# Performance work log

Hardware: AMD Instinct MI355X
Metric: run time of the kernel (lower is better)

The kernel has to match this reference:

```python
import jax, jax.numpy as jnp
import numpy as np
from jax import lax

Z_MAX = 0.3
WAVELENGTHS = jnp.array([0.65, 0.53, 0.47], jnp.float32)
LUMA = jnp.array([0.299, 0.587, 0.114], jnp.float32)


def conv2d(x, w, b):
    # x: (B,C,H,W), w: (O,I,kh,kw), SAME padding, stride 1
    y = lax.conv_general_dilated(x, w, (1, 1), 'SAME',
                                 dimension_numbers=('NCHW', 'OIHW', 'NCHW'))
    return y + b[None, :, None, None]


def group_norm(x, g, b, eps=1e-5):
    # GroupNorm(num_groups=1): normalize over (C,H,W) per sample
    mu = x.mean(axis=(1, 2, 3), keepdims=True)
    var = ((x - mu) ** 2).mean(axis=(1, 2, 3), keepdims=True)
    xn = (x - mu) * lax.rsqrt(var + eps)
    return xn * g[None, :, None, None] + b[None, :, None, None]


def setup_inputs() -> dict:
    key = jax.random.key(0)
    ks = jax.random.split(key, 16)
    B, C, H, W = 8, 3, 512, 512
    PH, ZH, MH = 16, 16, 32
    s = 0.1
    inp = {
        'x': jax.random.uniform(ks[0], (B, C, H, W), jnp.float32),
        'norm_g': jnp.ones((C,), jnp.float32), 'norm_b': jnp.zeros((C,), jnp.float32),
        'ph_w1': jax.random.normal(ks[1], (PH, C, 3, 3), jnp.float32) * s,
        'ph_b1': jnp.zeros((PH,), jnp.float32),
        'ph_w2': jax.random.normal(ks[2], (C, PH, 3, 3), jnp.float32) * s,
        'ph_b2': jnp.zeros((C,), jnp.float32),
        'z_w1': jax.random.normal(ks[3], (ZH, C, 3, 3), jnp.float32) * s,
        'z_b1': jnp.zeros((ZH,), jnp.float32),
        'z_w2': jax.random.normal(ks[4], (C, ZH, 3, 3), jnp.float32) * s,
        'z_b2': jnp.zeros((C,), jnp.float32),
        'freq_gain': jax.random.normal(ks[5], (C,), jnp.float32) * 0.01,
        'mix_w1': jax.random.normal(ks[6], (MH, C + 2, 3, 3), jnp.float32) * s,
        'mix_b1': jnp.zeros((MH,), jnp.float32),
        'gn1_g': jnp.ones((MH,), jnp.float32), 'gn1_b': jnp.zeros((MH,), jnp.float32),
        'mix_w2': jax.random.normal(ks[7], (MH, MH, 3, 3), jnp.float32) * s,
        'mix_b2': jnp.zeros((MH,), jnp.float32),
        'gn2_g': jnp.ones((MH,), jnp.float32), 'gn2_b': jnp.zeros((MH,), jnp.float32),
        'mix_w3': jax.random.normal(ks[8], (C, MH, 1, 1), jnp.float32) * s,
        'mix_b3': jnp.zeros((C,), jnp.float32),
        'se_w1': jax.random.normal(ks[9], (4, C), jnp.float32) * s,   # mid = max(3//4,4)=4
        'se_b1': jnp.zeros((4,), jnp.float32),
        'se_w2': jax.random.normal(ks[10], (C, 4), jnp.float32) * s,
        'se_b2': jnp.zeros((C,), jnp.float32),
        'alpha': jnp.asarray(0.3, jnp.float32),
    }
    return inp


def reference(x, norm_g, norm_b, ph_w1, ph_b1, ph_w2, ph_b2,
              z_w1, z_b1, z_w2, z_b2, freq_gain,
              mix_w1, mix_b1, gn1_g, gn1_b, mix_w2, mix_b2, gn2_g, gn2_b,
              mix_w3, mix_b3, se_w1, se_b1, se_w2, se_b2, alpha):
    B, C, H, W = x.shape
    # 1) norm
    xn = group_norm(x, norm_g, norm_b)
    # 2) phase prediction (small CNN, phi in [-pi, pi])
    h = jax.nn.silu(conv2d(xn, ph_w1, ph_b1))
    phi = jnp.tanh(conv2d(h, ph_w2, ph_b2)) * jnp.pi
    # 3) per-pixel propagation distance z in [0, z_max]
    hz = jax.nn.silu(conv2d(xn, z_w1, z_b1))
    z = jax.nn.sigmoid(conv2d(hz, z_w2, z_b2)) * Z_MAX
    # 4) complex field U0 = amp * exp(i*phi)  (amp_mode='identity')
    U0 = lax.complex(x * jnp.cos(phi), x * jnp.sin(phi))
    # 5) ASM propagation. kz = 2*pi*sqrt(1/lam^2 - fx^2 - fy^2), per-channel wavelength.
    fy = jnp.fft.fftfreq(H).astype(jnp.float32)
    fx = jnp.fft.fftfreq(W).astype(jnp.float32)
    f2 = fy[:, None] ** 2 + fx[None, :] ** 2                     # (H,W)
    inv_l2 = (1.0 / WAVELENGTHS ** 2)[:, None, None]             # (3,1,1)
    kz = 2.0 * jnp.pi * jnp.sqrt(jnp.maximum(inv_l2 - f2[None], 0.0))  # (3,H,W)
    # spatially varying z: base propagation at mean z + spatial phase correction
    z_mean = z.mean(axis=(2, 3), keepdims=True)                  # (B,3,1,1)
    Uf = jnp.fft.fft2(U0)
    Uf = Uf * (1.0 + freq_gain)[None, :, None, None].astype(Uf.dtype)  # FreqEnhance gain
    hp = kz[None] * z_mean                                       # (B,3,H,W)
    Uz = jnp.fft.ifft2(Uf * lax.complex(jnp.cos(hp), jnp.sin(hp)))
    k0 = (2.0 * jnp.pi / WAVELENGTHS)[None, :, None, None]
    cp = k0 * (z - z_mean)
    Uz = Uz * lax.complex(jnp.cos(cp), jnp.sin(cp))
    # 6) J = |Uz| with clamped sqrt
    J = jnp.sqrt(jnp.maximum(Uz.real ** 2 + Uz.imag ** 2, 1e-12))
    # 7) mix head: [x, J_luma, J_contrast] -> delta
    lw = LUMA[None, :, None, None]
    x_l = (x * lw).sum(axis=1, keepdims=True)
    J_l = (J * lw).sum(axis=1, keepdims=True)
    mix_in = jnp.concatenate([x, J_l, J_l - x_l], axis=1)        # (B,5,H,W)
    d = jax.nn.silu(group_norm(conv2d(mix_in, mix_w1, mix_b1), gn1_g, gn1_b))
    d = jax.nn.silu(group_norm(conv2d(d, mix_w2, mix_b2), gn2_g, gn2_b))
    delta = conv2d(d, mix_w3, mix_b3)                            # (B,3,H,W)
    # 8) SE channel attention
    p = delta.mean(axis=(2, 3))                                  # (B,3)
    wse = jax.nn.sigmoid(jax.nn.silu(p @ se_w1.T + se_b1) @ se_w2.T + se_b2)
    delta = delta * wse[:, :, None, None]
    # 9) residual update
    return x + alpha * delta
```

## Files before the change

### kernel.cpp

```cpp
#include <hip/hip_runtime.h>
#include <hip/hip_bf16.h>
#include <math.h>

#define DINL __device__ __forceinline__

namespace {
constexpr int Bn = 8, Cn = 3, Hn = 512, Wn = 512;
constexpr int HW  = Hn * Wn;
constexpr int CHW = Cn * HW;
constexpr float GEPS = 1e-5f;
constexpr float PIf  = 3.14159265358979323846f;

constexpr size_t OFF_RED = 0;
constexpr size_t OFF_PHI = 512;
constexpr size_t OFF_U   = OFF_PHI + (size_t)Bn * CHW * 2;
constexpr size_t OFF_J   = OFF_U   + (size_t)Bn * CHW * 4;
constexpr size_t OFF_D   = OFF_J   + (size_t)Bn * CHW * 2;
constexpr size_t OFF_Y2  = OFF_D   + (size_t)Bn * CHW * 2;
constexpr size_t OFF_W1B = OFF_Y2  + (size_t)Bn * 32 * HW;
constexpr size_t OFF_W2F = OFF_W1B + 3072 * 2;
constexpr size_t OFF_WH1 = OFF_W2F + 9216;
constexpr size_t OFF_WP2 = OFF_WH1 + 4608 * 2;
constexpr size_t OFF_WZ2 = OFF_WP2 + 4608;
constexpr size_t OFF_PRM = OFF_WZ2 + 4608;
constexpr size_t OFF_PART= OFF_PRM + 160 * 4;
constexpr size_t OFF_TW  = OFF_PART + 81920 * 4;
constexpr int PZ = 0;
constexpr int PG1 = 24576;
constexpr int PG2 = 40960;
constexpr int PD  = 57344;
}

typedef __bf16 bfx8 __attribute__((ext_vector_type(8)));
typedef float  fx4  __attribute__((ext_vector_type(4)));
typedef float  fx2  __attribute__((ext_vector_type(2)));

DINL float frcp(float a) { return __builtin_amdgcn_rcpf(a); }
DINL float sigm(float a) { return frcp(1.f + __expf(-a)); }
DINL float siluf(float a) { return a * frcp(1.f + __expf(-a)); }
DINL float ftanh(float a) { return 1.f - 2.f * frcp(1.f + __expf(2.f * a)); }
DINL unsigned short f2bf(float f) {
    unsigned u = __float_as_uint(f);
    return (unsigned short)((u + 0x7FFFu + ((u >> 16) & 1u)) >> 16);
}
DINL float bf2f(unsigned short h) {
    return __uint_as_float(((unsigned)h) << 16);
}
DINL unsigned short t1(float a) { return (unsigned short)(__float_as_uint(a) >> 16); }
DINL unsigned t2(float a, float b) {
    return (__float_as_uint(a) >> 16) | (__float_as_uint(b) & 0xFFFF0000u);
}
DINL unsigned char f2f8(float v) {
    return (unsigned char)(__builtin_amdgcn_cvt_pk_fp8_f32(v, v, 0, false) & 0xFF);
}
DINL unsigned short pk8(float a, float b) {
    return (unsigned short)(__builtin_amdgcn_cvt_pk_fp8_f32(a, b, 0, false) & 0xFFFF);
}
DINL unsigned pk4f8(float a, float b, float c, float d) {
    unsigned u = __builtin_amdgcn_cvt_pk_fp8_f32(a, b, 0, false);
    u = __builtin_amdgcn_cvt_pk_fp8_f32(c, d, u, true);
    return u;
}
template<int SEL>
DINL float f8f(unsigned u) { return __builtin_amdgcn_cvt_f32_fp8(u, SEL); }
DINL unsigned pkh(float a, float b) {
    auto h = __builtin_amdgcn_cvt_pkrtz(a, b);
    unsigned u; __builtin_memcpy(&u, &h, 4); return u;
}
DINL float2 uph(unsigned u) {
    _Float16 h[2]; __builtin_memcpy(h, &u, 4);
    return make_float2((float)h[0], (float)h[1]);
}
DINL unsigned short f2h(float a) {
    _Float16 h = (_Float16)a; unsigned short s; __builtin_memcpy(&s, &h, 2); return s;
}
DINL float h2f(unsigned short s) {
    _Float16 h; __builtin_memcpy(&h, &s, 2); return (float)h;
}

DINL int SW(int e) { return e ^ ((e >> 4) & 7); }

DINL float blockReduceSum(float v) {
    __shared__ float sm[4];
    int lane = threadIdx.x & 63, wid = threadIdx.x >> 6;
    #pragma unroll
    for (int o = 32; o > 0; o >>= 1) v += __shfl_down(v, o, 64);
    __syncthreads();
    if (lane == 0) sm[wid] = v;
    __syncthreads();
    if (wid == 0) {
        float r = (lane < 4) ? sm[lane] : 0.f;
        r += __shfl_down(r, 2, 64);
        r += __shfl_down(r, 1, 64);
        return r;
    }
    return 0.f;
}

DINL void blockReduceSum3(float& a, float& b, float& c) {
    __shared__ float sm3[12];
    int lane = threadIdx.x & 63, wid = threadIdx.x >> 6;
    #pragma unroll
    for (int o = 32; o > 0; o >>= 1) {
        a += __shfl_down(a, o, 64);
        b += __shfl_down(b, o, 64);
        c += __shfl_down(c, o, 64);
    }
    __syncthreads();
    if (lane == 0) { sm3[wid] = a; sm3[4 + wid] = b; sm3[8 + wid] = c; }
    __syncthreads();
    if (threadIdx.x == 0) {
        a = sm3[0] + sm3[1] + sm3[2] + sm3[3];
        b = sm3[4] + sm3[5] + sm3[6] + sm3[7];
        c = sm3[8] + sm3[9] + sm3[10] + sm3[11];
    }
}

__global__ __launch_bounds__(256) void k_init(
    const float* __restrict__ w1, const float* __restrict__ w2,
    const float* __restrict__ phw1, const float* __restrict__ zw1,
    const float* __restrict__ phw2, const float* __restrict__ zw2,
    const float* __restrict__ g2g, const float* __restrict__ g2b,
    const float* __restrict__ w3,
    unsigned short* __restrict__ w1bf, unsigned char* __restrict__ w2f8,
    unsigned short* __restrict__ wh1, unsigned char* __restrict__ wp2,
    unsigned char* __restrict__ wz2, float* __restrict__ prm,
    float2* __restrict__ gtw,
    const float* __restrict__ x, float* __restrict__ part)
{
    if (blockIdx.x < 36) {
        int i = blockIdx.x * 256 + threadIdx.x;
        if (i < 3072) {
            int o = i / 96, k = i - o * 96;
            int ky = k >> 5, r = k & 31, kx = r >> 3, c = r & 7;
            float v = 0.f;
            if (kx < 3 && c < 4) {
                float base = w1[o * 45 + c * 9 + ky * 3 + kx];
                float w4   = w1[o * 45 + 4 * 9 + ky * 3 + kx];
                v = (c == 3) ? base + w4
                  : base - ((c == 0) ? 0.299f : (c == 1) ? 0.587f : 0.114f) * w4;
            }
            w1bf[i] = f2bf(v);
        }
        if (i < 9216) {
            int tap = i >> 10, rr = i & 1023, row = rr >> 5, ci = rr & 31;
            int n = row & 15, hi = row >> 4;
            int ch = (n >> 2) * 8 + hi * 4 + (n & 3);
            w2f8[i] = f2f8(w2[ch * 288 + ci * 9 + tap]);
        }
        if (i < 4608) {
            int o = i / 96, k = i - o * 96;
            int ky = k >> 5, r = k & 31, kx = r >> 3, c = r & 7;
            float v = 0.f;
            if (kx < 3 && c < 3)
                v = (o < 16) ? phw1[o * 27 + c * 9 + ky * 3 + kx]
                             : zw1[(o - 16) * 27 + c * 9 + ky * 3 + kx];
            wh1[i] = f2bf(v);
        }
        if (i < 4608) {
            int tap = i / 512, rr = i - tap * 512, n = rr >> 5, k = rr & 31;
            float vp = (n < 3 && k < 16) ? phw2[n * 144 + k * 9 + tap] : 0.f;
            float vz = (n < 3) ? zw2[n * 288 + k * 9 + tap] : 0.f;
            wp2[i] = f2f8(vp);
            wz2[i] = f2f8(vz);
        }
        if (i < 160) {
            if (i < 32) {
                prm[i] = g2g[i];
            } else if (i < 64) {
                prm[i] = g2b[i - 32];
            } else {
                int j = (i - 64) & 31, c = (i - 64) >> 5;
                prm[i] = w3[c * 32 + j];
            }
        }
        return;
    }
    if (blockIdx.x == 36) {
        for (int i = threadIdx.x; i < 512; i += 256) {
            float s, c; __sincosf(-2.f * PIf * (float)i * (1.f / 512.f), &s, &c);
            gtw[i] = make_float2(c, s);
        }
        return;
    }
    const int bid = blockIdx.x - 37;
    const int b = bid >> 5, blk = bid & 31;
    const float4* xv = (const float4*)(x + (size_t)b * CHW + (size_t)blk * (CHW / 32));
    float s = 0.f, ss = 0.f;
    for (int i = threadIdx.x; i < (CHW / 32) / 4; i += 256) {
        float4 v = xv[i];
        s  += v.x + v.y + v.z + v.w;
        ss += v.x * v.x + v.y * v.y + v.z * v.z + v.w * v.w;
    }
    float rs = blockReduceSum(s);
    float rss = blockReduceSum(ss);
    if (threadIdx.x == 0) {
        part[PG1 + b * 64 + blk] = rs;
        part[PG1 + b * 64 + 32 + blk] = rss;
    }
}

__global__ __launch_bounds__(256) void k_heads(
    const float* __restrict__ x,
    const float* __restrict__ ng, const float* __restrict__ nb,
    const unsigned short* __restrict__ wh1,
    const float* __restrict__ phb1, const float* __restrict__ zb1,
    const unsigned char* __restrict__ wp2, const unsigned char* __restrict__ wz2,
    const float* __restrict__ phb2, const float* __restrict__ zb2,
    unsigned short* __restrict__ phi, float* __restrict__ part)
{
    const int tx0 = blockIdx.x * 16, ty0 = blockIdx.y * 16, b = blockIdx.z;
    const int local = blockIdx.y * 32 + blockIdx.x;
    const bool edge = (blockIdx.x == 0) || (blockIdx.x == 31) ||
                      (blockIdx.y == 0) || (blockIdx.y == 31);
    __shared__ unsigned short mt8[20 * 21 * 8];
    __shared__ __attribute__((aligned(16))) unsigned char ht8[324 * 48];
    __shared__ float xst[2];
    const int t = threadIdx.x;
    {
        const float* px = part + PG1 + (size_t)b * 64;
        float sv  = (t < 32) ? px[t] : 0.f;
        float ssv = (t >= 32 && t < 64) ? px[t] : 0.f;
        float r0 = blockReduceSum(sv);
        float r1 = blockReduceSum(ssv);
        if (t == 0) { xst[0] = r0; xst[1] = r1; }
        __syncthreads();
    }
    const float mu = xst[0] * (1.f / CHW);
    const float rsv = rsqrtf(xst[1] * (1.f / CHW) - mu * mu + GEPS);
    float sc[3], sh[3];
    #pragma unroll
    for (int c = 0; c < 3; ++c) { sc[c] = rsv * ng[c]; sh[c] = nb[c] - mu * rsv * ng[c]; }
    if (edge) {
        for (int e = t; e < 20 * 21; e += 256) {
            int yy = e / 21, xx = e - yy * 21;
            int gy = ty0 - 2 + yy, gx = tx0 - 2 + xx;
            float v0 = 0, v1 = 0, v2 = 0;
            if (xx < 20 && (unsigned)gy < (unsigned)Hn && (unsigned)gx < (unsigned)Wn) {
                size_t p = (size_t)b * CHW + (size_t)gy * Wn + gx;
                v0 = x[p] * sc[0] + sh[0];
                v1 = x[p + HW] * sc[1] + sh[1];
                v2 = x[p + 2 * HW] * sc[2] + sh[2];
            }
            *(uint4*)(mt8 + e * 8) = make_uint4(t2(v0, v1), (unsigned)t1(v2), 0u, 0u);
        }
    } else {
        for (int e = t; e < 20 * 21; e += 256) {
            int yy = e / 21, xx = e - yy * 21;
            float v0 = 0, v1 = 0, v2 = 0;
            if (xx < 20) {
                size_t p = (size_t)b * CHW + (size_t)(ty0 - 2 + yy) * Wn + (tx0 - 2 + xx);
                v0 = x[p] * sc[0] + sh[0];
                v1 = x[p + HW] * sc[1] + sh[1];
                v2 = x[p + 2 * HW] * sc[2] + sh[2];
            }
            *(uint4*)(mt8 + e * 8) = make_uint4(t2(v0, v1), (unsigned)t1(v2), 0u, 0u);
        }
    }
    const int wv = t >> 6, lane = t & 63, ln = lane & 15, q = lane >> 4;
    bfx8 Bf[3][3];
    #pragma unroll
    for (int ks = 0; ks < 3; ++ks)
        #pragma unroll
        for (int nt = 0; nt < 3; ++nt)
            Bf[ks][nt] = *(const bfx8*)(wh1 + (nt * 16 + ln) * 96 + ks * 32 + q * 8);
    float bph[4], bz0[4], bz1[4];
    #pragma unroll
    for (int r = 0; r < 4; ++r) {
        int ch = q * 4 + r;
        bph[r] = phb1[ch]; bz0[r] = zb1[ch]; bz1[r] = zb1[16 + ch];
    }
    __syncthreads();
    for (int mt = wv; mt < 21; mt += 4) {
        int p = mt * 16 + ln; if (p > 323) p = 323;
        const int hy = p / 18, hx = p - hy * 18;
        fx4 a0 = {0,0,0,0}, a1 = {0,0,0,0}, a2 = {0,0,0,0};
        #pragma unroll
        for (int ks = 0; ks < 3; ++ks) {
            bfx8 A = *(const bfx8*)(mt8 + ((hy + ks) * 21 + hx + q) * 8);
            a0 = __builtin_amdgcn_mfma_f32_16x16x32_bf16(Bf[ks][0], A, a0, 0, 0, 0);
            a1 = __builtin_amdgcn_mfma_f32_16x16x32_bf16(Bf[ks][1], A, a1, 0, 0, 0);
            a2 = __builtin_amdgcn_mfma_f32_16x16x32_bf16(Bf[ks][2], A, a2, 0, 0, 0);
        }
        bool live = true;
        if (edge) {
            const int gy = ty0 - 1 + hy, gx = tx0 - 1 + hx;
            live = (unsigned)gy < (unsigned)Hn && (unsigned)gx < (unsigned)Wn;
        }
        unsigned d0 = pk4f8(siluf(a0[0] + bph[0]), siluf(a0[1] + bph[1]),
                            siluf(a0[2] + bph[2]), siluf(a0[3] + bph[3]));
        unsigned d1 = pk4f8(siluf(a1[0] + bz0[0]), siluf(a1[1] + bz0[1]),
                            siluf(a1[2] + bz0[2]), siluf(a1[3] + bz0[3]));
        unsigned d2 = pk4f8(siluf(a2[0] + bz1[0]), siluf(a2[1] + bz1[1]),
                            siluf(a2[2] + bz1[2]), siluf(a2[3] + bz1[3]));
        if (!live) { d0 = 0u; d1 = 0u; d2 = 0u; }
        unsigned* hp = (unsigned*)(ht8 + p * 48 + q * 4);
        hp[0] = d0; hp[4] = d1; hp[8] = d2;
    }
    __syncthreads();
    fx4 accp[4], accz[4];
    #pragma unroll
    for (int i = 0; i < 4; ++i) { accp[i] = fx4{0,0,0,0}; accz[i] = fx4{0,0,0,0}; }
    #pragma unroll
    for (int tap = 0; tap < 9; ++tap) {
        const int ky = tap / 3, kx = tap - ky * 3;
        long Bp = *(const long*)(wp2 + tap * 512 + ln * 32 + q * 8);
        long Bz = *(const long*)(wz2 + tap * 512 + ln * 32 + q * 8);
        #pragma unroll
        for (int i = 0; i < 4; ++i) {
            const int oy = wv * 4 + i;
            const unsigned char* ap = ht8 + ((oy + ky) * 18 + ln + kx) * 48;
            long Ap = *(const long*)(ap + q * 8);
            long Az = *(const long*)(ap + 16 + q * 8);
            accp[i] = __builtin_amdgcn_mfma_f32_16x16x32_fp8_fp8(Ap, Bp, accp[i], 0, 0, 0);
            accz[i] = __builtin_amdgcn_mfma_f32_16x16x32_fp8_fp8(Az, Bz, accz[i], 0, 0, 0);
        }
    }
    __syncthreads();
    float* phs = (float*)ht8;
    float* zs  = phs + 1024;
    if (ln < 3) {
        #pragma unroll
        for (int i = 0; i < 4; ++i)
            #pragma unroll
            for (int r = 0; r < 4; ++r) {
                int pl = (wv * 4 + i) * 16 + q * 4 + r;
                phs[pl * 4 + ln] = accp[i][r];
                zs [pl * 4 + ln] = accz[i][r];
            }
    }
    asm volatile("" ::: "memory");
    float4 pv = ((const float4*)phs)[t];
    float4 zv = ((const float4*)zs)[t];
    const int gy = ty0 + (t >> 4), gx = tx0 + (t & 15);
    size_t pp = (size_t)b * CHW + (size_t)gy * Wn + gx;
    phi[pp]          = f2h(ftanh(pv.x + phb2[0]) * PIf);
    phi[pp + HW]     = f2h(ftanh(pv.y + phb2[1]) * PIf);
    phi[pp + 2 * HW] = f2h(ftanh(pv.z + phb2[2]) * PIf);
    float z0 = sigm(zv.x + zb2[0]) * 0.3f;
    float z1 = sigm(zv.y + zb2[1]) * 0.3f;
    float z2 = sigm(zv.z + zb2[2]) * 0.3f;
    blockReduceSum3(z0, z1, z2);
    if (t == 0) {
        part[PZ + (size_t)(b * 3 + 0) * 1024 + local] = z0;
        part[PZ + (size_t)(b * 3 + 1) * 1024 + local] = z1;
        part[PZ + (size_t)(b * 3 + 2) * 1024 + local] = z2;
    }
}

template<bool INV>
DINL float2* fft512_wave4(float2* a, float2* b, const float2* tw, int l)
{
    float2* src = a; float2* dst = b;
    int s = 1;
    #pragma unroll
    for (int st = 0; st < 4; ++st) {
        #pragma unroll
        for (int h = 0; h < 2; ++h) {
            const int i = l + h * 64;
            const int q = i & (s - 1);
            const int sm = i - q;
            const int si = SW(i);
            float2 A = src[si], B = src[si + 128], C = src[si + 256], D = src[si + 384];
            float t0x = A.x + C.x, t0y = A.y + C.y;
            float t1x = A.x - C.x, t1y = A.y - C.y;
            float t2x = B.x + D.x, t2y = B.y + D.y;
            float t3x = B.x - D.x, t3y = B.y - D.y;
            float i3x = INV ? -t3y : t3y;
            float i3y = INV ? t3x : -t3x;
            float u0x = t0x + t2x, u0y = t0y + t2y;
            float u2x = t0x - t2x, u2y = t0y - t2y;
            float u1x = t1x + i3x, u1y = t1y + i3y;
            float u3x = t1x - i3x, u3y = t1y - i3y;
            float2 w1 = tw[SW(sm)], w2 = tw[SW(2 * sm)], w3 = tw[SW(3 * sm)];
            float w1y = INV ? -w1.y : w1.y;
            float w2y = INV ? -w2.y : w2.y;
            float w3y = INV ? -w3.y : w3.y;
            const int base = q + 4 * sm;
            dst[SW(base)]         = make_float2(u0x, u0y);
            dst[SW(base + s)]     = make_float2(u1x * w1.x - u1y * w1y, u1x * w1y + u1y * w1.x);
            dst[SW(base + 2 * s)] = make_float2(u2x * w2.x - u2y * w2y, u2x * w2y + u2y * w2.x);
            dst[SW(base + 3 * s)] = make_float2(u3x * w3.x - u3y * w3y, u3x * w3y + u3y * w3.x);
        }
        float2* tmp = src; src = dst; dst = tmp;
        s <<= 2;
        asm volatile("" ::: "memory");
    }
    #pragma unroll
    for (int h = 0; h < 4; ++h) {
        const int j = l + h * 64;
        const int sj = SW(j);
        float2 u = src[sj], v = src[sj + 256];
        dst[sj]       = make_float2(u.x + v.x, u.y + v.y);
        dst[sj + 256] = make_float2(u.x - v.x, u.y - v.y);
    }
    float2* tmp = src; src = dst; dst = tmp;
    asm volatile("" ::: "memory");
    return src;
}

__global__ __launch_bounds__(256) void k_fftA(
    const float* __restrict__ x, const unsigned short* __restrict__ phi,
    unsigned* __restrict__ U, const float2* __restrict__ gtw)
{
    __shared__ float2 buf[4][2][512];
    __shared__ float2 tw[512];
    const int t = threadIdx.x, wv = t >> 6, l = t & 63;
    #pragma unroll
    for (int i = t; i < 512; i += 256) tw[SW(i)] = gtw[i];
    __syncthreads();
    const size_t line = (size_t)blockIdx.x * 4 + wv;
    const float* xr = x + line * 512;
    const unsigned short* pr = phi + line * 512;
    float2* A = buf[wv][0];
    float2* B = buf[wv][1];
    #pragma unroll
    for (int i = l; i < 512; i += 64) {
        float s, c; __sincosf(h2f(pr[i]), &s, &c);
        float xv = xr[i];
        A[SW(i)] = make_float2(xv * c, xv * s);
    }
    asm volatile("" ::: "memory");
    float2* res = fft512_wave4<false>(A, B, tw, l);
    unsigned* Ur = U + line * 512;
    #pragma unroll
    for (int i = l; i < 512; i += 64) {
        float2 v = res[SW(i)];
        Ur[i] = pkh(v.x, v.y);
    }
}

__global__ __launch_bounds__(256) void k_transpose(unsigned* __restrict__ U,
                                                   const float* __restrict__ part,
                                                   float* __restrict__ red)
{
    const int img = blockIdx.y;
    if (blockIdx.x == 0) {
        float4 a4 = ((const float4*)(part + PZ + (size_t)img * 1024))[threadIdx.x];
        float r = blockReduceSum(a4.x + a4.y + a4.z + a4.w);
        if (threadIdx.x == 0) red[16 + img] = r;
    }
    int rem = blockIdx.x, ti = 0;
    while (rem >= 8 - ti) { rem -= 8 - ti; ++ti; }
    const int tj = ti + rem;
    unsigned* Ub = U + (size_t)img * HW;
    __shared__ unsigned ta[64][65];
    __shared__ unsigned tb[64][65];
    const int t = threadIdx.x;
    const int cc = t & 63, r0 = t >> 6;
    const int ar = ti * 64, ac = tj * 64;
    #pragma unroll
    for (int k = 0; k < 16; ++k) {
        int r = r0 + k * 4;
        ta[r][cc] = Ub[(size_t)(ar + r) * 512 + ac + cc];
    }
    if (ti != tj) {
        #pragma unroll
        for (int k = 0; k < 16; ++k) {
            int r = r0 + k * 4;
            tb[r][cc] = Ub[(size_t)(ac + r) * 512 + ar + cc];
        }
    }
    __syncthreads();
    #pragma unroll
    for (int k = 0; k < 16; ++k) {
        int r = r0 + k * 4;
        Ub[(size_t)(ac + r) * 512 + ar + cc] = ta[cc][r];
    }
    if (ti != tj) {
        #pragma unroll
        for (int k = 0; k < 16; ++k) {
            int r = r0 + k * 4;
            Ub[(size_t)(ar + r) * 512 + ac + cc] = tb[cc][r];
        }
    }
}

__global__ __launch_bounds__(256) void k_fftB(
    unsigned* __restrict__ U, const float* __restrict__ red,
    const float* __restrict__ fgain, const float2* __restrict__ gtw)
{
    __shared__ float2 buf[4][2][512];
    __shared__ float2 tw[512];
    const int t = threadIdx.x, wv = t >> 6, l = t & 63;
    #pragma unroll
    for (int i = t; i < 512; i += 256) tw[SW(i)] = gtw[i];
    const int line = blockIdx.x * 4 + wv;
    const int bc = line >> 9;
    const int fw = line & 511;
    const int c = bc % 3;
    const float zm = red[16 + bc] * (1.f / HW);
    __syncthreads();
    unsigned* Ur = U + (size_t)line * 512;
    float2* A = buf[wv][0];
    float2* B = buf[wv][1];
    #pragma unroll
    for (int i = l; i < 512; i += 64) A[SW(i)] = uph(Ur[i]);
    asm volatile("" ::: "memory");
    float2* res = fft512_wave4<false>(A, B, tw, l);
    const float gain = 1.f + fgain[c];
    const float lam  = (c == 0) ? 0.65f : (c == 1) ? 0.53f : 0.47f;
    const float il2  = 1.f / (lam * lam);
    const float fwv  = (float)(fw < 256 ? fw : fw - 512) * (1.f / 512.f);
    const float f2w  = fwv * fwv;
    #pragma unroll
    for (int i = l; i < 512; i += 64) {
        float fh = (float)(i < 256 ? i : i - 512) * (1.f / 512.f);
        float kz = 2.f * PIf * sqrtf(fmaxf(il2 - f2w - fh * fh, 0.f));
        float sn, cs; __sincosf(kz * zm, &sn, &cs);
        const int si = SW(i);
        float2 v = res[si];
        res[si] = make_float2(gain * (v.x * cs - v.y * sn), gain * (v.x * sn + v.y * cs));
    }
    asm volatile("" ::: "memory");
    float2* other = (res == A) ? B : A;
    float2* res2 = fft512_wave4<true>(res, other, tw, l);
    #pragma unroll
    for (int i = l; i < 512; i += 64) {
        float2 v = res2[SW(i)];
        Ur[i] = pkh(v.x * (1.f / 512.f), v.y * (1.f / 512.f));
    }
}

__global__ __launch_bounds__(256) void k_fftC(
    const unsigned* __restrict__ U, unsigned short* __restrict__ J,
    const float2* __restrict__ gtw)
{
    __shared__ float2 buf[4][2][512];
    __shared__ float2 tw[512];
    const int t = threadIdx.x, wv = t >> 6, l = t & 63;
    #pragma unroll
    for (int i = t; i < 512; i += 256) tw[SW(i)] = gtw[i];
    __syncthreads();
    const size_t line = (size_t)blockIdx.x * 4 + wv;
    const unsigned* Ur = U + line * 512;
    float2* A = buf[wv][0];
    float2* B = buf[wv][1];
    #pragma unroll
    for (int i = l; i < 512; i += 64) A[SW(i)] = uph(Ur[i]);
    asm volatile("" ::: "memory");
    float2* res = fft512_wave4<true>(A, B, tw, l);
    unsigned short* Jr = J + line * 512;
    #pragma unroll
    for (int i = l; i < 512; i += 64) {
        float2 v = res[SW(i)];
        float re = v.x * (1.f / 512.f), im = v.y * (1.f / 512.f);
        Jr[i] = f2h(sqrtf(fmaxf(re * re + im * im, 1e-12f)));
    }
}

__global__ __launch_bounds__(256) void k_m1(
    const float* __restrict__ x, const unsigned short* __restrict__ Jb,
    const unsigned short* __restrict__ w1bf, const float* __restrict__ b1,
    float* __restrict__ part)
{
    const int tx0 = blockIdx.x * 32, ty0 = blockIdx.y * 32, b = blockIdx.z;
    const int local = blockIdx.y * 16 + blockIdx.x;
    const bool edge = (blockIdx.x == 0) || (blockIdx.x == 15) ||
                      (blockIdx.y == 0) || (blockIdx.y == 15);
    __shared__ unsigned short mt8[34 * 35 * 8];
    const int t = threadIdx.x;
    for (int e = t; e < 34 * 35; e += 256) {
        int yy = e / 35, xx = e - yy * 35;
        int gy = ty0 - 1 + yy, gx = tx0 - 1 + xx;
        float v0 = 0, v1 = 0, v2 = 0, jl = 0;
        bool ok = edge ? (xx < 34 && (unsigned)gy < (unsigned)Hn && (unsigned)gx < (unsigned)Wn)
                       : (xx < 34);
        if (ok) {
            size_t p = (size_t)b * CHW + (size_t)gy * Wn + gx;
            v0 = x[p]; v1 = x[p + HW]; v2 = x[p + 2 * HW];
            jl = 0.299f * h2f(Jb[p]) + 0.587f * h2f(Jb[p + HW]) + 0.114f * h2f(Jb[p + 2 * HW]);
        }
        *(uint4*)(mt8 + e * 8) = make_uint4(t2(v0, v1), t2(v2, jl), 0u, 0u);
    }
    __syncthreads();
    const int wv = t >> 6, lane = t & 63, ln = lane & 15, q = lane >> 4;
    bfx8 Bf[3][2];
    #pragma unroll
    for (int ks = 0; ks < 3; ++ks)
        #pragma unroll
        for (int nt = 0; nt < 2; ++nt)
            Bf[ks][nt] = *(const bfx8*)(w1bf + (nt * 16 + ln) * 96 + ks * 32 + q * 8);
    const float b1v0 = b1[ln], b1v1 = b1[16 + ln];
    float s = 0.f, ss = 0.f;
    for (int g = wv; g < 64; g += 4) {
        const int row = g >> 1, ct = (g & 1) * 16;
        fx4 a0 = {0.f, 0.f, 0.f, 0.f}, a1 = {0.f, 0.f, 0.f, 0.f};
        #pragma unroll
        for (int ks = 0; ks < 3; ++ks) {
            bfx8 A = *(const bfx8*)(mt8 + ((row + ks) * 35 + ct + ln + q) * 8);
            a0 = __builtin_amdgcn_mfma_f32_16x16x32_bf16(A, Bf[ks][0], a0, 0, 0, 0);
            a1 = __builtin_amdgcn_mfma_f32_16x16x32_bf16(A, Bf[ks][1], a1, 0, 0, 0);
        }
        #pragma unroll
        for (int r = 0; r < 4; ++r) {
            float u0 = a0[r] + b1v0, u1 = a1[r] + b1v1;
            s += u0 + u1; ss += u0 * u0 + u1 * u1;
        }
    }
    float rs = blockReduceSum(s);
    float rss = blockReduceSum(ss);
    if (t == 0) {
        part[PG1 + (size_t)b * 1024 + local] = rs;
        part[PG1 + (size_t)(8 + b) * 1024 + local] = rss;
    }
}

__global__ __launch_bounds__(256) void k_m2(
    const float* __restrict__ x, const unsigned short* __restrict__ Jb,
    const unsigned short* __restrict__ w1bf, const float* __restrict__ b1,
    const float* __restrict__ g1g, const float* __restrict__ g1b,
    const unsigned char* __restrict__ w2f8, const float* __restrict__ b2,
    float* __restrict__ part, unsigned char* __restrict__ y2)
{
    const int tx0 = blockIdx.x * 16, ty0 = blockIdx.y * 16, b = blockIdx.z;
    const int local = blockIdx.y * 32 + blockIdx.x;
    const bool edge = (blockIdx.x == 0) || (blockIdx.x == 31) ||
                      (blockIdx.y == 0) || (blockIdx.y == 31);
    __shared__ unsigned short mt8[20 * 21 * 8];
    __shared__ __attribute__((aligned(16))) unsigned char dt2[324 * 40];
    __shared__ float g1s[2];
    const int t = threadIdx.x;
    {
        float4 a4 = make_float4(0.f, 0.f, 0.f, 0.f), c4v = a4;
        if (t < 64) {
            a4  = ((const float4*)(part + PG1 + (size_t)b * 1024))[t];
            c4v = ((const float4*)(part + PG1 + (size_t)(8 + b) * 1024))[t];
        }
        float r0 = blockReduceSum(a4.x + a4.y + a4.z + a4.w);
        float r1 = blockReduceSum(c4v.x + c4v.y + c4v.z + c4v.w);
        if (t == 0) { g1s[0] = r0; g1s[1] = r1; }
        __syncthreads();
    }
    const float mu1 = g1s[0] * (1.f / (32.f * HW));
    const float rs1 = rsqrtf(g1s[1] * (1.f / (32.f * HW)) - mu1 * mu1 + GEPS);
    for (int e = t; e < 20 * 21; e += 256) {
        int yy = e / 21, xx = e - yy * 21;
        int gy = ty0 - 2 + yy, gx = tx0 - 2 + xx;
        float v0 = 0, v1 = 0, v2 = 0, jl = 0;
        bool ok = edge ? (xx < 20 && (unsigned)gy < (unsigned)Hn && (unsigned)gx < (unsigned)Wn)
                       : (xx < 20);
        if (ok) {
            size_t p = (size_t)b * CHW + (size_t)gy * Wn + gx;
            v0 = x[p]; v1 = x[p + HW]; v2 = x[p + 2 * HW];
            jl = 0.299f * h2f(Jb[p]) + 0.587f * h2f(Jb[p + HW]) + 0.114f * h2f(Jb[p + 2 * HW]);
        }
        *(uint4*)(mt8 + e * 8) = make_uint4(t2(v0, v1), t2(v2, jl), 0u, 0u);
    }
    const int wv = t >> 6, lane = t & 63, ln = lane & 15, q = lane >> 4;
    float scv[2][4], ofv[2][4];
    #pragma unroll
    for (int g = 0; g < 2; ++g)
        #pragma unroll
        for (int r = 0; r < 4; ++r) {
            int ch = g * 16 + q * 4 + r;
            float sg = rs1 * g1g[ch];
            scv[g][r] = sg;
            ofv[g][r] = (b1[ch] - mu1) * sg + g1b[ch];
        }
    bfx8 Bf[3][2];
    #pragma unroll
    for (int ks = 0; ks < 3; ++ks)
        #pragma unroll
        for (int nt = 0; nt < 2; ++nt)
            Bf[ks][nt] = *(const bfx8*)(w1bf + (nt * 16 + ln) * 96 + ks * 32 + q * 8);
    __syncthreads();
    for (int mt = wv; mt < 21; mt += 4) {
        int p = mt * 16 + ln; if (p > 323) p = 323;
        const int hy = p / 18, hx = p - hy * 18;
        fx4 a0 = {0.f, 0.f, 0.f, 0.f}, a1 = {0.f, 0.f, 0.f, 0.f};
        #pragma unroll
        for (int ks = 0; ks < 3; ++ks) {
            bfx8 A = *(const bfx8*)(mt8 + ((hy + ks) * 21 + hx + q) * 8);
            a0 = __builtin_amdgcn_mfma_f32_16x16x32_bf16(Bf[ks][0], A, a0, 0, 0, 0);
            a1 = __builtin_amdgcn_mfma_f32_16x16x32_bf16(Bf[ks][1], A, a1, 0, 0, 0);
        }
        bool live = true;
        if (edge) {
            const int gy = ty0 - 1 + hy, gx = tx0 - 1 + hx;
            live = (unsigned)gy < (unsigned)Hn && (unsigned)gx < (unsigned)Wn;
        }
        unsigned d0 = pk4f8(siluf(a0[0] * scv[0][0] + ofv[0][0]),
                            siluf(a0[1] * scv[0][1] + ofv[0][1]),
                            siluf(a0[2] * scv[0][2] + ofv[0][2]),
                            siluf(a0[3] * scv[0][3] + ofv[0][3]));
        unsigned d1 = pk4f8(siluf(a1[0] * scv[1][0] + ofv[1][0]),
                            siluf(a1[1] * scv[1][1] + ofv[1][1]),
                            siluf(a1[2] * scv[1][2] + ofv[1][2]),
                            siluf(a1[3] * scv[1][3] + ofv[1][3]));
        if (!live) { d0 = 0u; d1 = 0u; }
        unsigned* dp = (unsigned*)(dt2 + p * 40 + q * 4);
        dp[0] = d0; dp[4] = d1;
    }
    __syncthreads();
    fx4 c2[4][2];
    #pragma unroll
    for (int i = 0; i < 4; ++i)
        #pragma unroll
        for (int nt = 0; nt < 2; ++nt)
            c2[i][nt] = fx4{0.f, 0.f, 0.f, 0.f};
    #pragma unroll
    for (int tap = 0; tap < 9; ++tap) {
        const int ky = tap / 3, kx = tap - ky * 3;
        long B0 = *(const long*)(w2f8 + tap * 1024 + ln * 32 + q * 8);
        long B1 = *(const long*)(w2f8 + tap * 1024 + (16 + ln) * 32 + q * 8);
        #pragma unroll
        for (int i = 0; i < 4; ++i) {
            const int oy = wv * 4 + i;
            long A = *(const long*)(dt2 + ((oy + ky) * 18 + ln + kx) * 40 + q * 8);
            c2[i][0] = __builtin_amdgcn_mfma_f32_16x16x32_fp8_fp8(B0, A, c2[i][0], 0, 0, 0);
            c2[i][1] = __builtin_amdgcn_mfma_f32_16x16x32_fp8_fp8(B1, A, c2[i][1], 0, 0, 0);
        }
    }
    float bv[2][4];
    #pragma unroll
    for (int nt = 0; nt < 2; ++nt)
        #pragma unroll
        for (int r = 0; r < 4; ++r)
            bv[nt][r] = b2[q * 8 + nt * 4 + r];
    float s = 0.f, ss = 0.f;
    const int gxo = tx0 + ln;
    #pragma unroll
    for (int i = 0; i < 4; ++i) {
        const int gy = ty0 + wv * 4 + i;
        size_t base = ((size_t)b * HW + (size_t)gy * Wn + gxo) * 32 + q * 8;
        float v0 = c2[i][0][0] + bv[0][0], v1 = c2[i][0][1] + bv[0][1];
        float v2 = c2[i][0][2] + bv[0][2], v3 = c2[i][0][3] + bv[0][3];
        float w0 = c2[i][1][0] + bv[1][0], w1 = c2[i][1][1] + bv[1][1];
        float w2 = c2[i][1][2] + bv[1][2], w3 = c2[i][1][3] + bv[1][3];
        s  += v0 + v1 + v2 + v3 + w0 + w1 + w2 + w3;
        ss += v0 * v0 + v1 * v1 + v2 * v2 + v3 * v3
            + w0 * w0 + w1 * w1 + w2 * w2 + w3 * w3;
        unsigned lo = pk4f8(v0, v1, v2, v3);
        unsigned hi = pk4f8(w0, w1, w2, w3);
        unsigned long long pk = (unsigned long long)lo | ((unsigned long long)hi << 32);
        *(unsigned long long*)(y2 + base) = pk;
    }
    float rsum = blockReduceSum(s);
    float rss = blockReduceSum(ss);
    if (t == 0) {
        part[PG2 + (size_t)b * 1024 + local] = rsum;
        part[PG2 + (size_t)(8 + b) * 1024 + local] = rss;
    }
}

__global__ __launch_bounds__(256) void k_m3(
    const unsigned char* __restrict__ y2,
    const float* __restrict__ prm, const float* __restrict__ b3,
    unsigned short* __restrict__ dl, float* __restrict__ part)
{
    const int t = threadIdx.x;
    const int b = blockIdx.x >> 7;
    const int local = blockIdx.x & 127;
    __shared__ float g2s[2];
    __shared__ float lut[8192];
    {
        float4 a4 = ((const float4*)(part + PG2 + (size_t)b * 1024))[t];
        float4 c4 = ((const float4*)(part + PG2 + (size_t)(8 + b) * 1024))[t];
        float r0 = blockReduceSum(a4.x + a4.y + a4.z + a4.w);
        float r1 = blockReduceSum(c4.x + c4.y + c4.z + c4.w);
        if (t == 0) { g2s[0] = r0; g2s[1] = r1; }
        __syncthreads();
    }
    const float mu = g2s[0] * (1.f / (32.f * HW));
    const float rs = rsqrtf(g2s[1] * (1.f / (32.f * HW)) - mu * mu + GEPS);
    for (int e = t; e < 8192; e += 256) {
        int j = e >> 8;
        float v = f8f<0>((unsigned)(e & 255));
        lut[e] = siluf((v - mu) * rs * prm[j] + prm[32 + j]);
    }
    __syncthreads();
    const float bb0 = b3[0], bb1 = b3[1], bb2 = b3[2];
    float s0 = 0.f, s1 = 0.f, s2 = 0.f;
    #pragma unroll
    for (int k = 0; k < 8; ++k) {
        int idx = blockIdx.x * 2048 + k * 256 + t;
        int pix = idx & (HW - 1);
        const uint4* yp = (const uint4*)(y2 + (size_t)idx * 32);
        uint4 L0 = yp[0], L1 = yp[1];
        unsigned Lw[8] = {L0.x, L0.y, L0.z, L0.w, L1.x, L1.y, L1.z, L1.w};
        float a0 = bb0, a1 = bb1, a2 = bb2;
        #pragma unroll
        for (int w = 0; w < 8; ++w) {
            unsigned u = Lw[w];
            #pragma unroll
            for (int h = 0; h < 4; ++h) {
                int j = w * 4 + h;
                int code = (int)((u >> (8 * h)) & 255u);
                float sv = lut[j * 256 + code];
                a0 += sv * prm[64 + j]; a1 += sv * prm[96 + j]; a2 += sv * prm[128 + j];
            }
        }
        size_t p = (size_t)b * CHW + pix;
        dl[p] = f2h(a0); dl[p + HW] = f2h(a1); dl[p + 2 * HW] = f2h(a2);
        s0 += a0; s1 += a1; s2 += a2;
    }
    blockReduceSum3(s0, s1, s2);
    if (t == 0) {
        part[PD + (size_t)(b * 3 + 0) * 1024 + local] = s0;
        part[PD + (size_t)(b * 3 + 1) * 1024 + local] = s1;
        part[PD + (size_t)(b * 3 + 2) * 1024 + local] = s2;
    }
}

__global__ __launch_bounds__(256) void k_fin(
    const float* __restrict__ part, float* __restrict__ red,
    const float* __restrict__ w1, const float* __restrict__ b1,
    const float* __restrict__ w2, const float* __restrict__ b2,
    const float* __restrict__ alpha)
{
    __shared__ float sm[24];
    const int t = threadIdx.x, wv = t >> 6, l = t & 63;
    for (int g = wv; g < 24; g += 4) {
        const float* p = part + PD + (size_t)g * 1024;
        float s = p[l] + p[l + 64];
        #pragma unroll
        for (int o = 32; o > 0; o >>= 1) s += __shfl_down(s, o, 64);
        if (l == 0) sm[g] = s;
    }
    __syncthreads();
    if (t < 8) {
        int b = t;
        float p0 = sm[b * 3 + 0] * (1.f / HW);
        float p1 = sm[b * 3 + 1] * (1.f / HW);
        float p2 = sm[b * 3 + 2] * (1.f / HW);
        float h[4];
        #pragma unroll
        for (int j = 0; j < 4; ++j) {
            float a = b1[j] + p0 * w1[j * 3] + p1 * w1[j * 3 + 1] + p2 * w1[j * 3 + 2];
            h[j] = siluf(a);
        }
        float al = alpha[0];
        #pragma unroll
        for (int c = 0; c < 3; ++c) {
            float a = b2[c] + h[0] * w2[c * 4] + h[1] * w2[c * 4 + 1]
                            + h[2] * w2[c * 4 + 2] + h[3] * w2[c * 4 + 3];
            red[96 + b * 3 + c] = al * sigm(a);
        }
    }
}

__global__ __launch_bounds__(256) void k_out(
    const float* __restrict__ x, const unsigned short* __restrict__ dl,
    const float* __restrict__ red, float* __restrict__ out)
{
    int i = blockIdx.x * 256 + threadIdx.x;
    float aw = red[96 + (i >> 16)];
    float4 xv = ((const float4*)x)[i];
    uint2 dv2 = ((const uint2*)dl)[i];
    float2 d01 = uph(dv2.x);
    float2 d23 = uph(dv2.y);
    float4 o;
    o.x = xv.x + aw * d01.x; o.y = xv.y + aw * d01.y;
    o.z = xv.z + aw * d23.x; o.w = xv.w + aw * d23.y;
    ((float4*)out)[i] = o;
}

extern "C" void kernel_launch(void* const* d_in, const int* in_sizes, int n_in,
                              void* d_out, int out_size, void* d_ws, size_t ws_size,
                              hipStream_t stream)
{
    const float* x     = (const float*)d_in[0];
    const float* ng    = (const float*)d_in[1];
    const float* nb    = (const float*)d_in[2];
    const float* ph_w1 = (const float*)d_in[3];
    const float* ph_b1 = (const float*)d_in[4];
    const float* ph_w2 = (const float*)d_in[5];
    const float* ph_b2 = (const float*)d_in[6];
    const float* z_w1  = (const float*)d_in[7];
    const float* z_b1  = (const float*)d_in[8];
    const float* z_w2  = (const float*)d_in[9];
    const float* z_b2  = (const float*)d_in[10];
    const float* fgain = (const float*)d_in[11];
    const float* mw1   = (const float*)d_in[12];
    const float* mb1   = (const float*)d_in[13];
    const float* g1g   = (const float*)d_in[14];
    const float* g1b   = (const float*)d_in[15];
    const float* mw2   = (const float*)d_in[16];
    const float* mb2   = (const float*)d_in[17];
    const float* g2g   = (const float*)d_in[18];
    const float* g2b   = (const float*)d_in[19];
    const float* mw3   = (const float*)d_in[20];
    const float* mb3   = (const float*)d_in[21];
    const float* sw1   = (const float*)d_in[22];
    const float* sb1   = (const float*)d_in[23];
    const float* sw2   = (const float*)d_in[24];
    const float* sb2   = (const float*)d_in[25];
    const float* alpha = (const float*)d_in[26];

    char* ws = (char*)d_ws;
    float*  red = (float*)(ws + OFF_RED);
    unsigned short* phi = (unsigned short*)(ws + OFF_PHI);
    unsigned* U = (unsigned*)(ws + OFF_U);
    unsigned short* Jb = (unsigned short*)(ws + OFF_J);
    unsigned short* dl = (unsigned short*)(ws + OFF_D);
    unsigned char*  y2   = (unsigned char*)(ws + OFF_Y2);
    unsigned short* w1bf = (unsigned short*)(ws + OFF_W1B);
    unsigned char*  w2f8 = (unsigned char*)(ws + OFF_W2F);
    unsigned short* wh1  = (unsigned short*)(ws + OFF_WH1);
    unsigned char*  wp2  = (unsigned char*)(ws + OFF_WP2);
    unsigned char*  wz2  = (unsigned char*)(ws + OFF_WZ2);
    float* prm  = (float*)(ws + OFF_PRM);
    float* part = (float*)(ws + OFF_PART);
    float2* gtw = (float2*)(ws + OFF_TW);
    float* out = (float*)d_out;

    hipLaunchKernelGGL(k_init, dim3(293), dim3(256), 0, stream,
                       mw1, mw2, ph_w1, z_w1, ph_w2, z_w2, g2g, g2b, mw3,
                       w1bf, w2f8, wh1, wp2, wz2, prm, gtw, x, part);
    hipLaunchKernelGGL(k_heads, dim3(32, 32, 8), dim3(256), 0, stream,
                       x, ng, nb, wh1, ph_b1, z_b1, wp2, wz2, ph_b2, z_b2, phi, part);
    hipLaunchKernelGGL(k_fftA, dim3(3072), dim3(256), 0, stream, x, phi, U, gtw);
    hipLaunchKernelGGL(k_transpose, dim3(36, 24), dim3(256), 0, stream, U, part, red);
    hipLaunchKernelGGL(k_fftB, dim3(3072), dim3(256), 0, stream, U, red, fgain, gtw);
    hipLaunchKernelGGL(k_transpose, dim3(36, 24), dim3(256), 0, stream, U, part, red);
    hipLaunchKernelGGL(k_fftC, dim3(3072), dim3(256), 0, stream, U, Jb, gtw);
    hipLaunchKernelGGL(k_m1, dim3(16, 16, 8), dim3(256), 0, stream, x, Jb, w1bf, mb1, part);
    hipLaunchKernelGGL(k_m2, dim3(32, 32, 8), dim3(256), 0, stream,
                       x, Jb, w1bf, mb1, g1g, g1b, w2f8, mb2, part, y2);
    hipLaunchKernelGGL(k_m3, dim3(1024), dim3(256), 0, stream, y2, prm, mb3, dl, part);
    hipLaunchKernelGGL(k_fin, dim3(1), dim3(256), 0, stream, part, red, sw1, sb1, sw2, sb2, alpha);
    hipLaunchKernelGGL(k_out, dim3(6144), dim3(256), 0, stream, x, dl, red, out);
}
```

Baseline: 449.2 us.

## Fuse FFT transposes into row-FFT kernels via shared-memory slabs

Removes the two standalone in-place transpose kernels. k_fftA now runs 16 rows per block, stages results in a shared slab, and writes them transposed to U with 16-byte stores. k_fftC reads a transposed 16-column slab before its row FFTs. The aim is to cut two full read/write passes over U and two launches. In exchange, grids shrink to 768 blocks, shared memory per block grows (lower occupancy), and each wave now runs four sequential FFTs.

New measurement: 457.0 us. No clear change (+1.7%).

```diff
diff --git a/kernel.cpp b/kernel.cpp
--- a/kernel.cpp
+++ b/kernel.cpp
@@ -401,78 +401,53 @@
 
 __global__ __launch_bounds__(256) void k_fftA(
     const float* __restrict__ x, const unsigned short* __restrict__ phi,
-    unsigned* __restrict__ U, const float2* __restrict__ gtw)
+    unsigned* __restrict__ U, const float2* __restrict__ gtw,
+    const float* __restrict__ part, float* __restrict__ red)
 {
     __shared__ float2 buf[4][2][512];
     __shared__ float2 tw[512];
+    __shared__ unsigned oslab[16][516];
     const int t = threadIdx.x, wv = t >> 6, l = t & 63;
-    #pragma unroll
+    const int img = blockIdx.y;
+    const int r0  = blockIdx.x * 16;
     for (int i = t; i < 512; i += 256) tw[SW(i)] = gtw[i];
-    __syncthreads();
-    const size_t line = (size_t)blockIdx.x * 4 + wv;
-    const float* xr = x + line * 512;
-    const unsigned short* pr = phi + line * 512;
+    if (blockIdx.x == 0) {
+        float4 a4 = ((const float4*)(part + PZ + (size_t)img * 1024))[t];
+        float r = blockReduceSum(a4.x + a4.y + a4.z + a4.w);
+        if (t == 0) red[16 + img] = r;
+    }
+    __syncthreads();
     float2* A = buf[wv][0];
     float2* B = buf[wv][1];
     #pragma unroll
-    for (int i = l; i < 512; i += 64) {
-        float s, c; __sincosf(h2f(pr[i]), &s, &c);
-        float xv = xr[i];
-        A[SW(i)] = make_float2(xv * c, xv * s);
-    }
-    asm volatile("" ::: "memory");
-    float2* res = fft512_wave4<false>(A, B, tw, l);
-    unsigned* Ur = U + line * 512;
-    #pragma unroll
-    for (int i = l; i < 512; i += 64) {
-        float2 v = res[SW(i)];
-        Ur[i] = pkh(v.x, v.y);
-    }
-}
-
-__global__ __launch_bounds__(256) void k_transpose(unsigned* __restrict__ U,
-                                                   const float* __restrict__ part,
-                                                   float* __restrict__ red)
-{
-    const int img = blockIdx.y;
-    if (blockIdx.x == 0) {
-        float4 a4 = ((const float4*)(part + PZ + (size_t)img * 1024))[threadIdx.x];
-        float r = blockReduceSum(a4.x + a4.y + a4.z + a4.w);
-        if (threadIdx.x == 0) red[16 + img] = r;
-    }
-    int rem = blockIdx.x, ti = 0;
-    while (rem >= 8 - ti) { rem -= 8 - ti; ++ti; }
-    const int tj = ti + rem;
-    unsigned* Ub = U + (size_t)img * HW;
-    __shared__ unsigned ta[64][65];
-    __shared__ unsigned tb[64][65];
-    const int t = threadIdx.x;
-    const int cc = t & 63, r0 = t >> 6;
-    const int ar = ti * 64, ac = tj * 64;
-    #pragma unroll
-    for (int k = 0; k < 16; ++k) {
-        int r = r0 + k * 4;
-        ta[r][cc] = Ub[(size_t)(ar + r) * 512 + ac + cc];
-    }
-    if (ti != tj) {
-        #pragma unroll
-        for (int k = 0; k < 16; ++k) {
-            int r = r0 + k * 4;
-            tb[r][cc] = Ub[(size_t)(ac + r) * 512 + ar + cc];
-        }
-    }
-    __syncthreads();
-    #pragma unroll
-    for (int k = 0; k < 16; ++k) {
-        int r = r0 + k * 4;
-        Ub[(size_t)(ac + r) * 512 + ar + cc] = ta[cc][r];
-    }
-    if (ti != tj) {
-        #pragma unroll
-        for (int k = 0; k < 16; ++k) {
-            int r = r0 + k * 4;
-            Ub[(size_t)(ar + r) * 512 + ac + cc] = tb[cc][r];
-        }
+    for (int li = 0; li < 4; ++li) {
+        const int lrow = wv + 4 * li;
+        const size_t line = (size_t)img * 512 + r0 + lrow;
+        const float* xr = x + line * 512;
+        const unsigned short* pr = phi + line * 512;
+        for (int i = l; i < 512; i += 64) {
+            float s, c; __sincosf(h2f(pr[i]), &s, &c);
+            float xv = xr[i];
+            A[SW(i)] = make_float2(xv * c, xv * s);
+        }
+        asm volatile("" ::: "memory");
+        float2* res = fft512_wave4<false>(A, B, tw, l);
+        for (int i = l; i < 512; i += 64) {
+            float2 v = res[SW(i)];
+            oslab[lrow][i] = pkh(v.x, v.y);
+        }
+        asm volatile("" ::: "memory");
+    }
+    __syncthreads();
+    unsigned* UT = U + (size_t)img * HW;
+    for (int j = t; j < 512; j += 256) {
+        unsigned g[16];
+        #pragma unroll
+        for (int k = 0; k < 16; ++k) g[k] = oslab[k][j];
+        unsigned* dst = UT + (size_t)j * 512 + r0;
+        #pragma unroll
+        for (int k = 0; k < 4; ++k)
+            ((uint4*)dst)[k] = make_uint4(g[4*k], g[4*k+1], g[4*k+2], g[4*k+3]);
     }
 }
 
@@ -528,24 +503,39 @@
 {
     __shared__ float2 buf[4][2][512];
     __shared__ float2 tw[512];
+    __shared__ unsigned islab[16][516];
     const int t = threadIdx.x, wv = t >> 6, l = t & 63;
-    #pragma unroll
+    const int img = blockIdx.y;
+    const int r0  = blockIdx.x * 16;
     for (int i = t; i < 512; i += 256) tw[SW(i)] = gtw[i];
-    __syncthreads();
-    const size_t line = (size_t)blockIdx.x * 4 + wv;
-    const unsigned* Ur = U + line * 512;
+    const unsigned* UT = U + (size_t)img * HW;
+    for (int j = t; j < 512; j += 256) {
+        const unsigned* src = UT + (size_t)j * 512 + r0;
+        #pragma unroll
+        for (int k = 0; k < 4; ++k) {
+            uint4 g = ((const uint4*)src)[k];
+            islab[4*k + 0][j] = g.x;
+            islab[4*k + 1][j] = g.y;
+            islab[4*k + 2][j] = g.z;
+            islab[4*k + 3][j] = g.w;
+        }
+    }
+    __syncthreads();
     float2* A = buf[wv][0];
     float2* B = buf[wv][1];
     #pragma unroll
-    for (int i = l; i < 512; i += 64) A[SW(i)] = uph(Ur[i]);
-    asm volatile("" ::: "memory");
-    float2* res = fft512_wave4<true>(A, B, tw, l);
-    unsigned short* Jr = J + line * 512;
-    #pragma unroll
-    for (int i = l; i < 512; i += 64) {
-        float2 v = res[SW(i)];
-        float re = v.x * (1.f / 512.f), im = v.y * (1.f / 512.f);
-        Jr[i] = f2h(sqrtf(fmaxf(re * re + im * im, 1e-12f)));
+    for (int li = 0; li < 4; ++li) {
+        const int lrow = wv + 4 * li;
+        for (int i = l; i < 512; i += 64) A[SW(i)] = uph(islab[lrow][i]);
+        asm volatile("" ::: "memory");
+        float2* res = fft512_wave4<true>(A, B, tw, l);
+        unsigned short* Jr = J + ((size_t)img * 512 + r0 + lrow) * 512;
+        for (int i = l; i < 512; i += 64) {
+            float2 v = res[SW(i)];
+            float re = v.x * (1.f / 512.f), im = v.y * (1.f / 512.f);
+            Jr[i] = f2h(sqrtf(fmaxf(re * re + im * im, 1e-12f)));
+        }
+        asm volatile("" ::: "memory");
     }
 }
 
@@ -910,11 +900,9 @@
                        w1bf, w2f8, wh1, wp2, wz2, prm, gtw, x, part);
     hipLaunchKernelGGL(k_heads, dim3(32, 32, 8), dim3(256), 0, stream,
                        x, ng, nb, wh1, ph_b1, z_b1, wp2, wz2, ph_b2, z_b2, phi, part);
-    hipLaunchKernelGGL(k_fftA, dim3(3072), dim3(256), 0, stream, x, phi, U, gtw);
-    hipLaunchKernelGGL(k_transpose, dim3(36, 24), dim3(256), 0, stream, U, part, red);
+    hipLaunchKernelGGL(k_fftA, dim3(32, 24), dim3(256), 0, stream, x, phi, U, gtw, part, red);
     hipLaunchKernelGGL(k_fftB, dim3(3072), dim3(256), 0, stream, U, red, fgain, gtw);
-    hipLaunchKernelGGL(k_transpose, dim3(36, 24), dim3(256), 0, stream, U, part, red);
-    hipLaunchKernelGGL(k_fftC, dim3(3072), dim3(256), 0, stream, U, Jb, gtw);
+    hipLaunchKernelGGL(k_fftC, dim3(32, 24), dim3(256), 0, stream, U, Jb, gtw);
     hipLaunchKernelGGL(k_m1, dim3(16, 16, 8), dim3(256), 0, stream, x, Jb, w1bf, mb1, part);
     hipLaunchKernelGGL(k_m2, dim3(32, 32, 8), dim3(256), 0, stream,
                        x, Jb, w1bf, mb1, g1g, g1b, w2f8, mb2, part, y2);
```
